# Optimization experiments

Hardware: AMD Instinct MI355X
Metric: run time of the kernel (lower is better)

## Reference

```python
import jax, jax.numpy as jnp
import numpy as np

ALPHA = 0.2  # LeakyReLU negative slope


def _pair_indices(N):
    # Faithful reproduction of the source's cat(dim=1)+view indexing quirk.
    # a_input[b, i, j, :F]  = h[b, idx(m0)] with m0 = 2*(i*N + j)
    # a_input[b, i, j, F:]  = h[b, idx(m1)] with m1 = m0 + 1
    # idx(m) = m // N            if m <  N*N   (first repeat: h_i blocks)
    #        = (m - N*N) % N     if m >= N*N   (second repeat: h_j tiling)
    i = jnp.arange(N, dtype=jnp.int32)[:, None]
    j = jnp.arange(N, dtype=jnp.int32)[None, :]
    m0 = 2 * (i * N + j)
    m1 = m0 + 1
    NN = N * N
    idx0 = jnp.where(m0 < NN, m0 // N, (m0 - NN) % N)
    idx1 = jnp.where(m1 < NN, m1 // N, (m1 - NN) % N)
    return idx0, idx1  # each [N, N] int32


def reference(inp, W, a):
    # inp: [B, N, Fin], W: [Fin, Fout], a: [2*Fout, 1]
    h = inp @ W                       # [B, N, F]
    B, N, F = h.shape
    a1 = a[:F, 0]                     # [F]
    a2 = a[F:, 0]                     # [F]
    # Decompose additive score: a_input @ a = a1.h_left + a2.h_right
    s1 = h @ a1                       # [B, N]
    s2 = h @ a2                       # [B, N]
    idx0, idx1 = _pair_indices(N)     # [N, N]
    score = s1[:, idx0] + s2[:, idx1]                     # [B, N, N]
    score = jax.nn.leaky_relu(score, negative_slope=ALPHA)
    attn = jax.nn.softmax(score, axis=1)                  # softmax over dim=1 as in source
    # dropout is identity in eval mode (dropout=0.0)
    h_prime = jnp.einsum('bij,bjf->bif', attn, h)         # [B, N, F]
    return jax.nn.elu(h_prime)                            # concat=True -> ELU


def setup_inputs() -> dict:
    B, N, Fin, Fout = 4, 4096, 128, 64
    key = jax.random.key(0)
    k1, k2, k3 = jax.random.split(key, 3)
    inp = jax.random.normal(k1, (B, N, Fin), dtype=jnp.float32)
    # xavier_uniform with gain=1.414
    gain = 1.414
    lim_W = gain * np.sqrt(6.0 / (Fin + Fout))
    W = jax.random.uniform(k2, (Fin, Fout), dtype=jnp.float32, minval=-lim_W, maxval=lim_W)
    lim_a = gain * np.sqrt(6.0 / (2 * Fout + 1))
    a = jax.random.uniform(k3, (2 * Fout, 1), dtype=jnp.float32, minval=-lim_a, maxval=lim_a)
    return {"inp": inp, "W": W, "a": a}
```

## Files before the change

kernel.cpp:

```cpp
#include <hip/hip_runtime.h>
#include <math.h>

#define ALPHA 0.2f

constexpr int BB   = 4;
constexpr int NN_  = 4096;
constexpr int HN   = 2048;
constexpr int FIN  = 128;
constexpr int FF   = 64;
constexpr int ROWS = BB * NN_;

constexpr size_t WS_H  = 0;
constexpr size_t WS_C  = (size_t)ROWS * FF;
constexpr size_t WS_E  = WS_C + ROWS;
constexpr size_t WS_A0 = WS_E + ROWS;
constexpr size_t WS_A1 = WS_A0 + (size_t)BB * FF;
constexpr size_t WS_U  = WS_A1 + (size_t)BB * FF;
constexpr size_t WS_M  = WS_U + (size_t)BB * FF;

__global__ __launch_bounds__(256) void k1_gemm(const float* __restrict__ inp,
                                               const float* __restrict__ W,
                                               const float* __restrict__ a,
                                               float* __restrict__ ws) {
  const int lane = threadIdx.x & 63;
  const int wv = __builtin_amdgcn_readfirstlane((int)(threadIdx.x >> 6));
  const int rowbase = blockIdx.x * 32 + wv * 8;

  float Wreg[FIN];
  #pragma unroll
  for (int k = 0; k < FIN; ++k) Wreg[k] = W[k * FF + lane];

  const float a1 = a[lane];
  const float a2 = a[FF + lane];
  const float asum = a1 + a2;

  float* hout = ws + WS_H;
  float* cout = ws + WS_C;
  float* eout = ws + WS_E;

  if (blockIdx.x == 0) {
    for (int t = threadIdx.x; t < 3 * BB * FF; t += 256) ws[WS_A0 + t] = 0.f;
  }

  for (int p = 0; p < 4; ++p) {
    const int r0 = rowbase + 2 * p;
    const float* p0 = inp + (size_t)r0 * FIN;
    const float* p1 = p0 + FIN;
    float h0a = 0.f, h0b = 0.f, h1a = 0.f, h1b = 0.f;
    #pragma unroll
    for (int k = 0; k < FIN; k += 2) {
      h0a = fmaf(p0[k],     Wreg[k],     h0a);
      h0b = fmaf(p0[k + 1], Wreg[k + 1], h0b);
      h1a = fmaf(p1[k],     Wreg[k],     h1a);
      h1b = fmaf(p1[k + 1], Wreg[k + 1], h1b);
    }
    const float h0 = h0a + h0b;
    const float h1 = h1a + h1b;
    hout[(size_t)r0 * FF + lane] = h0;
    hout[(size_t)(r0 + 1) * FF + lane] = h1;

    float c0 = h0 * asum, e0 = h0 * a1;
    float c1 = h1 * asum, e1 = h1 * a2;
    #pragma unroll
    for (int s = 32; s >= 1; s >>= 1) {
      c0 += __shfl_xor(c0, s, 64);
      e0 += __shfl_xor(e0, s, 64);
      c1 += __shfl_xor(c1, s, 64);
      e1 += __shfl_xor(e1, s, 64);
    }
    if (lane == 0) {
      cout[r0] = c0;     eout[r0] = e0;
      cout[r0 + 1] = c1; eout[r0 + 1] = e1;
    }
  }
}

constexpr int NSEG = 32;
constexpr int SEGR = 128;

__global__ __launch_bounds__(256) void k3_colsum(float* __restrict__ ws) {
  const int b   = blockIdx.x / NSEG;
  const int seg = blockIdx.x % NSEG;
  const int tid = threadIdx.x;
  const float* c = ws + WS_C + (size_t)b * NN_;
  const float* e = ws + WS_E + (size_t)b * NN_;
  const float* h = ws + WS_H + (size_t)b * NN_ * FF;

  __shared__ float lr_s[NN_];
  __shared__ float red[256];
  __shared__ float qbuf[SEGR];
  __shared__ float wbuf[SEGR];
  __shared__ float accbuf[4][2][64];

  float mymax = -INFINITY;
  for (int k = tid; k < NN_; k += 256) {
    float x = c[k];
    x = x > 0.f ? x : ALPHA * x;
    lr_s[k] = x;
    mymax = fmaxf(mymax, x);
  }
  red[tid] = mymax;
  __syncthreads();
  #pragma unroll
  for (int s = 128; s >= 2; s >>= 1) {
    if (tid < s) red[tid] = fmaxf(red[tid], red[tid + s]);
    __syncthreads();
  }
  const float M0 = red[0];
  const float M1 = red[1];
  __syncthreads();

  const float Mp = (tid & 1) ? M1 : M0;
  float mysum = 0.f;
  for (int k = tid; k < NN_; k += 256) mysum += __expf(lr_s[k] - Mp);
  red[tid] = mysum;
  __syncthreads();
  #pragma unroll
  for (int s = 128; s >= 2; s >>= 1) {
    if (tid < s) red[tid] += red[tid + s];
    __syncthreads();
  }
  const float P0 = red[0];
  const float P1 = red[1];

  if (tid < SEGR) {
    const int j  = seg * SEGR + tid;
    const int jp = j & (HN - 1);
    float d = e[2 * jp] + e[2 * jp + 1];
    float v = d > 0.f ? d : ALPHA * d;
    float Mt = (j < HN) ? M0 : M1;
    float Pt = (j < HN) ? P0 : P1;
    float m  = fmaxf(Mt, v);
    float eM = __expf(Mt - m);
    float ev = __expf(v - m);
    float Z  = eM * Pt + (float)HN * ev;
    qbuf[tid] = eM / Z;
    wbuf[tid] = ev / Z;
  }
  if (seg == 0 && tid == 0) {
    ws[WS_M + 2 * b]     = M0;
    ws[WS_M + 2 * b + 1] = M1;
  }
  __syncthreads();

  const int wv = tid >> 6;
  const int lane = tid & 63;
  float accA = 0.f, accU = 0.f;
  const int lbase = wv * (SEGR / 4);
  #pragma unroll 4
  for (int r = 0; r < SEGR / 4; ++r) {
    const int lj = lbase + r;
    const int j  = seg * SEGR + lj;
    float hv = h[(size_t)j * FF + lane];
    accA = fmaf(qbuf[lj], hv, accA);
    accU = fmaf(wbuf[lj], hv, accU);
  }
  accbuf[wv][0][lane] = accA;
  accbuf[wv][1][lane] = accU;
  __syncthreads();
  if (tid < 64) {
    float sA = accbuf[0][0][tid] + accbuf[1][0][tid] + accbuf[2][0][tid] + accbuf[3][0][tid];
    float sU = accbuf[0][1][tid] + accbuf[1][1][tid] + accbuf[2][1][tid] + accbuf[3][1][tid];
    float* A = ws + ((seg < NSEG / 2) ? WS_A0 : WS_A1) + (size_t)b * FF;
    atomicAdd(&A[tid], sA);
    atomicAdd(ws + WS_U + (size_t)b * FF + tid, sU);
  }
}

__global__ __launch_bounds__(256) void k4_out(const float* __restrict__ ws,
                                              float* __restrict__ out) {
  const int idx = blockIdx.x * 256 + threadIdx.x;
  const int b   = idx >> 16;
  const int rem = idx & 65535;
  const int i   = rem >> 4;
  const int fg  = rem & 15;
  float4 v;
  if (i < HN) {
    const float* c = ws + WS_C + (size_t)b * NN_;
    const float M0 = ws[WS_M + 2 * b];
    const float M1 = ws[WS_M + 2 * b + 1];
    float c0 = c[2 * i], c1 = c[2 * i + 1];
    c0 = c0 > 0.f ? c0 : ALPHA * c0;
    c1 = c1 > 0.f ? c1 : ALPHA * c1;
    const float al = __expf(c0 - M0);
    const float be = __expf(c1 - M1);
    const float4 A0v = reinterpret_cast<const float4*>(ws + WS_A0 + (size_t)b * FF)[fg];
    const float4 A1v = reinterpret_cast<const float4*>(ws + WS_A1 + (size_t)b * FF)[fg];
    v.x = al * A0v.x + be * A1v.x;
    v.y = al * A0v.y + be * A1v.y;
    v.z = al * A0v.z + be * A1v.z;
    v.w = al * A0v.w + be * A1v.w;
  } else {
    v = reinterpret_cast<const float4*>(ws + WS_U + (size_t)b * FF)[fg];
  }
  v.x = v.x > 0.f ? v.x : expm1f(v.x);
  v.y = v.y > 0.f ? v.y : expm1f(v.y);
  v.z = v.z > 0.f ? v.z : expm1f(v.z);
  v.w = v.w > 0.f ? v.w : expm1f(v.w);
  reinterpret_cast<float4*>(out)[idx] = v;
}

extern "C" void kernel_launch(void* const* d_in, const int* in_sizes, int n_in,
                              void* d_out, int out_size, void* d_ws, size_t ws_size,
                              hipStream_t stream) {
  (void)in_sizes; (void)n_in; (void)out_size; (void)ws_size;
  const float* inp = (const float*)d_in[0];
  const float* W   = (const float*)d_in[1];
  const float* a   = (const float*)d_in[2];
  float* out = (float*)d_out;
  float* ws  = (float*)d_ws;

  hipLaunchKernelGGL(k1_gemm,   dim3(ROWS / 32),        dim3(256), 0, stream, inp, W, a, ws);
  hipLaunchKernelGGL(k3_colsum, dim3(BB * NSEG),        dim3(256), 0, stream, ws);
  hipLaunchKernelGGL(k4_out,    dim3(ROWS * FF / 1024), dim3(256), 0, stream, ws, out);
}
```

Baseline: 36.47 us.

## Split softmax stats into dedicated kernel and stage GEMM rows in LDS

Adds a new k2_stats kernel, one block per batch, that computes the column max and sum statistics and the per-pair weight tables once, instead of every k3_colsum block recomputing them redundantly over 4096 entries. k3_colsum then only reads the precomputed weights and accumulates h. k1_gemm now loads its 32 input rows into shared memory with coalesced float4 loads and reads them as float4 broadcasts, rather than each lane reading the same global addresses. The cost is an extra kernel launch and a serial k2 stage running on only 4 blocks.

```diff
diff --git a/kernel.cpp b/kernel.cpp
--- a/kernel.cpp
+++ b/kernel.cpp
@@ -17,50 +17,62 @@
 constexpr size_t WS_A1 = WS_A0 + (size_t)BB * FF;
 constexpr size_t WS_U  = WS_A1 + (size_t)BB * FF;
 constexpr size_t WS_M  = WS_U + (size_t)BB * FF;
+constexpr size_t WS_WQ = WS_M + 2 * BB;
 
 __global__ __launch_bounds__(256) void k1_gemm(const float* __restrict__ inp,
                                                const float* __restrict__ W,
                                                const float* __restrict__ a,
                                                float* __restrict__ ws) {
-  const int lane = threadIdx.x & 63;
-  const int wv = __builtin_amdgcn_readfirstlane((int)(threadIdx.x >> 6));
-  const int rowbase = blockIdx.x * 32 + wv * 8;
+  const int tid  = threadIdx.x;
+  const int lane = tid & 63;
+  const int wv   = __builtin_amdgcn_readfirstlane(tid >> 6);
+  __shared__ float rows_s[32 * FIN];
 
   float Wreg[FIN];
   #pragma unroll
   for (int k = 0; k < FIN; ++k) Wreg[k] = W[k * FF + lane];
-
   const float a1 = a[lane];
   const float a2 = a[FF + lane];
   const float asum = a1 + a2;
 
+  const int rowbase = blockIdx.x * 32;
+  const float4* src = reinterpret_cast<const float4*>(inp + (size_t)rowbase * FIN);
+  float4* dst = reinterpret_cast<float4*>(rows_s);
+  #pragma unroll
+  for (int i = 0; i < 4; ++i) dst[tid + i * 256] = src[tid + i * 256];
+  __syncthreads();
+
   float* hout = ws + WS_H;
   float* cout = ws + WS_C;
   float* eout = ws + WS_E;
 
-  if (blockIdx.x == 0) {
-    for (int t = threadIdx.x; t < 3 * BB * FF; t += 256) ws[WS_A0 + t] = 0.f;
-  }
-
+  #pragma unroll
   for (int p = 0; p < 4; ++p) {
-    const int r0 = rowbase + 2 * p;
-    const float* p0 = inp + (size_t)r0 * FIN;
-    const float* p1 = p0 + FIN;
-    float h0a = 0.f, h0b = 0.f, h1a = 0.f, h1b = 0.f;
+    const int lr0 = wv * 8 + 2 * p;
+    const float* rp0 = rows_s + lr0 * FIN;
+    const float* rp1 = rp0 + FIN;
+    float h0 = 0.f, h0b = 0.f, h1 = 0.f, h1b = 0.f;
     #pragma unroll
-    for (int k = 0; k < FIN; k += 2) {
-      h0a = fmaf(p0[k],     Wreg[k],     h0a);
-      h0b = fmaf(p0[k + 1], Wreg[k + 1], h0b);
-      h1a = fmaf(p1[k],     Wreg[k],     h1a);
-      h1b = fmaf(p1[k + 1], Wreg[k + 1], h1b);
-    }
-    const float h0 = h0a + h0b;
-    const float h1 = h1a + h1b;
-    hout[(size_t)r0 * FF + lane] = h0;
-    hout[(size_t)(r0 + 1) * FF + lane] = h1;
-
-    float c0 = h0 * asum, e0 = h0 * a1;
-    float c1 = h1 * asum, e1 = h1 * a2;
+    for (int k = 0; k < FIN; k += 4) {
+      const float4 x0 = *reinterpret_cast<const float4*>(rp0 + k);
+      const float4 x1 = *reinterpret_cast<const float4*>(rp1 + k);
+      h0  = fmaf(x0.x, Wreg[k],     h0);
+      h0b = fmaf(x0.y, Wreg[k + 1], h0b);
+      h0  = fmaf(x0.z, Wreg[k + 2], h0);
+      h0b = fmaf(x0.w, Wreg[k + 3], h0b);
+      h1  = fmaf(x1.x, Wreg[k],     h1);
+      h1b = fmaf(x1.y, Wreg[k + 1], h1b);
+      h1  = fmaf(x1.z, Wreg[k + 2], h1);
+      h1b = fmaf(x1.w, Wreg[k + 3], h1b);
+    }
+    const float H0 = h0 + h0b;
+    const float H1 = h1 + h1b;
+    const int r0 = rowbase + lr0;
+    hout[(size_t)r0 * FF + lane] = H0;
+    hout[(size_t)(r0 + 1) * FF + lane] = H1;
+
+    float c0 = H0 * asum, e0 = H0 * a1;
+    float c1 = H1 * asum, e1 = H1 * a2;
     #pragma unroll
     for (int s = 32; s >= 1; s >>= 1) {
       c0 += __shfl_xor(c0, s, 64);
@@ -75,92 +87,111 @@
   }
 }
 
+__global__ __launch_bounds__(1024) void k2_stats(float* __restrict__ ws) {
+  const int b    = blockIdx.x;
+  const int tid  = threadIdx.x;
+  const int lane = tid & 63;
+  const int w    = tid >> 6;
+  const float* c = ws + WS_C + (size_t)b * NN_;
+  const float* e = ws + WS_E + (size_t)b * NN_;
+  __shared__ float redm[16][2];
+  __shared__ float bc[4];
+
+  const float4 cv = reinterpret_cast<const float4*>(c)[tid];
+  const float l0 = cv.x > 0.f ? cv.x : ALPHA * cv.x;
+  const float l1 = cv.y > 0.f ? cv.y : ALPHA * cv.y;
+  const float l2 = cv.z > 0.f ? cv.z : ALPHA * cv.z;
+  const float l3 = cv.w > 0.f ? cv.w : ALPHA * cv.w;
+  float me = fmaxf(l0, l2), mo = fmaxf(l1, l3);
+  #pragma unroll
+  for (int s = 32; s >= 1; s >>= 1) {
+    me = fmaxf(me, __shfl_xor(me, s, 64));
+    mo = fmaxf(mo, __shfl_xor(mo, s, 64));
+  }
+  if (lane == 0) { redm[w][0] = me; redm[w][1] = mo; }
+  __syncthreads();
+  if (tid == 0) {
+    float M0 = -INFINITY, M1 = -INFINITY;
+    for (int i = 0; i < 16; ++i) {
+      M0 = fmaxf(M0, redm[i][0]);
+      M1 = fmaxf(M1, redm[i][1]);
+    }
+    bc[0] = M0; bc[1] = M1;
+  }
+  __syncthreads();
+  const float M0 = bc[0], M1 = bc[1];
+  float se = __expf(l0 - M0) + __expf(l2 - M0);
+  float so = __expf(l1 - M1) + __expf(l3 - M1);
+  #pragma unroll
+  for (int s = 32; s >= 1; s >>= 1) {
+    se += __shfl_xor(se, s, 64);
+    so += __shfl_xor(so, s, 64);
+  }
+  __syncthreads();
+  if (lane == 0) { redm[w][0] = se; redm[w][1] = so; }
+  __syncthreads();
+  if (tid == 0) {
+    float P0 = 0.f, P1 = 0.f;
+    for (int i = 0; i < 16; ++i) { P0 += redm[i][0]; P1 += redm[i][1]; }
+    bc[2] = P0; bc[3] = P1;
+    ws[WS_M + 2 * b]     = M0;
+    ws[WS_M + 2 * b + 1] = M1;
+  }
+  __syncthreads();
+  const float P0 = bc[2], P1 = bc[3];
+
+  float4* wq = reinterpret_cast<float4*>(ws + WS_WQ) + (size_t)b * HN;
+  #pragma unroll
+  for (int i = 0; i < 2; ++i) {
+    const int jp = tid + i * 1024;
+    const float2 ev = reinterpret_cast<const float2*>(e)[jp];
+    const float d = ev.x + ev.y;
+    const float v = d > 0.f ? d : ALPHA * d;
+    const float m0 = fmaxf(M0, v), m1 = fmaxf(M1, v);
+    const float eM0 = __expf(M0 - m0), ev0 = __expf(v - m0);
+    const float eM1 = __expf(M1 - m1), ev1 = __expf(v - m1);
+    const float Z0 = eM0 * P0 + (float)HN * ev0;
+    const float Z1 = eM1 * P1 + (float)HN * ev1;
+    wq[jp] = make_float4(eM0 / Z0, ev0 / Z0, eM1 / Z1, ev1 / Z1);
+  }
+  if (tid < FF) {
+    ws[WS_A0 + (size_t)b * FF + tid] = 0.f;
+    ws[WS_A1 + (size_t)b * FF + tid] = 0.f;
+    ws[WS_U  + (size_t)b * FF + tid] = 0.f;
+  }
+}
+
 constexpr int NSEG = 32;
 constexpr int SEGR = 128;
 
 __global__ __launch_bounds__(256) void k3_colsum(float* __restrict__ ws) {
-  const int b   = blockIdx.x / NSEG;
-  const int seg = blockIdx.x % NSEG;
-  const int tid = threadIdx.x;
-  const float* c = ws + WS_C + (size_t)b * NN_;
-  const float* e = ws + WS_E + (size_t)b * NN_;
+  const int b    = blockIdx.x >> 5;
+  const int seg  = blockIdx.x & 31;
+  const int tid  = threadIdx.x;
+  const int lane = tid & 63;
+  const int wv   = __builtin_amdgcn_readfirstlane(tid >> 6);
   const float* h = ws + WS_H + (size_t)b * NN_ * FF;
-
-  __shared__ float lr_s[NN_];
-  __shared__ float red[256];
-  __shared__ float qbuf[SEGR];
-  __shared__ float wbuf[SEGR];
+  const float4* wq = reinterpret_cast<const float4*>(ws + WS_WQ) + (size_t)b * HN;
   __shared__ float accbuf[4][2][64];
 
-  float mymax = -INFINITY;
-  for (int k = tid; k < NN_; k += 256) {
-    float x = c[k];
-    x = x > 0.f ? x : ALPHA * x;
-    lr_s[k] = x;
-    mymax = fmaxf(mymax, x);
-  }
-  red[tid] = mymax;
-  __syncthreads();
-  #pragma unroll
-  for (int s = 128; s >= 2; s >>= 1) {
-    if (tid < s) red[tid] = fmaxf(red[tid], red[tid + s]);
-    __syncthreads();
-  }
-  const float M0 = red[0];
-  const float M1 = red[1];
-  __syncthreads();
-
-  const float Mp = (tid & 1) ? M1 : M0;
-  float mysum = 0.f;
-  for (int k = tid; k < NN_; k += 256) mysum += __expf(lr_s[k] - Mp);
-  red[tid] = mysum;
-  __syncthreads();
-  #pragma unroll
-  for (int s = 128; s >= 2; s >>= 1) {
-    if (tid < s) red[tid] += red[tid + s];
-    __syncthreads();
-  }
-  const float P0 = red[0];
-  const float P1 = red[1];
-
-  if (tid < SEGR) {
-    const int j  = seg * SEGR + tid;
-    const int jp = j & (HN - 1);
-    float d = e[2 * jp] + e[2 * jp + 1];
-    float v = d > 0.f ? d : ALPHA * d;
-    float Mt = (j < HN) ? M0 : M1;
-    float Pt = (j < HN) ? P0 : P1;
-    float m  = fmaxf(Mt, v);
-    float eM = __expf(Mt - m);
-    float ev = __expf(v - m);
-    float Z  = eM * Pt + (float)HN * ev;
-    qbuf[tid] = eM / Z;
-    wbuf[tid] = ev / Z;
-  }
-  if (seg == 0 && tid == 0) {
-    ws[WS_M + 2 * b]     = M0;
-    ws[WS_M + 2 * b + 1] = M1;
-  }
-  __syncthreads();
-
-  const int wv = tid >> 6;
-  const int lane = tid & 63;
+  const int j0 = seg * SEGR + wv * 32;
   float accA = 0.f, accU = 0.f;
-  const int lbase = wv * (SEGR / 4);
-  #pragma unroll 4
-  for (int r = 0; r < SEGR / 4; ++r) {
-    const int lj = lbase + r;
-    const int j  = seg * SEGR + lj;
-    float hv = h[(size_t)j * FF + lane];
-    accA = fmaf(qbuf[lj], hv, accA);
-    accU = fmaf(wbuf[lj], hv, accU);
+  #pragma unroll 8
+  for (int r = 0; r < 32; ++r) {
+    const int j = j0 + r;
+    const float hv = h[(size_t)j * FF + lane];
+    const float4 q = wq[j & (HN - 1)];
+    const float qa = (j < HN) ? q.x : q.z;
+    const float qu = (j < HN) ? q.y : q.w;
+    accA = fmaf(qa, hv, accA);
+    accU = fmaf(qu, hv, accU);
   }
   accbuf[wv][0][lane] = accA;
   accbuf[wv][1][lane] = accU;
   __syncthreads();
   if (tid < 64) {
-    float sA = accbuf[0][0][tid] + accbuf[1][0][tid] + accbuf[2][0][tid] + accbuf[3][0][tid];
-    float sU = accbuf[0][1][tid] + accbuf[1][1][tid] + accbuf[2][1][tid] + accbuf[3][1][tid];
+    const float sA = accbuf[0][0][tid] + accbuf[1][0][tid] + accbuf[2][0][tid] + accbuf[3][0][tid];
+    const float sU = accbuf[0][1][tid] + accbuf[1][1][tid] + accbuf[2][1][tid] + accbuf[3][1][tid];
     float* A = ws + ((seg < NSEG / 2) ? WS_A0 : WS_A1) + (size_t)b * FF;
     atomicAdd(&A[tid], sA);
     atomicAdd(ws + WS_U + (size_t)b * FF + tid, sU);
@@ -210,7 +241,8 @@
   float* out = (float*)d_out;
   float* ws  = (float*)d_ws;
 
-  hipLaunchKernelGGL(k1_gemm,   dim3(ROWS / 32),        dim3(256), 0, stream, inp, W, a, ws);
-  hipLaunchKernelGGL(k3_colsum, dim3(BB * NSEG),        dim3(256), 0, stream, ws);
-  hipLaunchKernelGGL(k4_out,    dim3(ROWS * FF / 1024), dim3(256), 0, stream, ws, out);
-}
+  hipLaunchKernelGGL(k1_gemm,   dim3(ROWS / 32),        dim3(256),  0, stream, inp, W, a, ws);
+  hipLaunchKernelGGL(k2_stats,  dim3(BB),               dim3(1024), 0, stream, ws);
+  hipLaunchKernelGGL(k3_colsum, dim3(BB * NSEG),        dim3(256),  0, stream, ws);
+  hipLaunchKernelGGL(k4_out,    dim3(ROWS * FF / 1024), dim3(256),  0, stream, ws, out);
+}
```

Result: faster. 34.99 us (-4.1%).
